# Kernel optimization log

Measured on AMD Instinct MI355X. Metric: run time of the kernel, lower is better.

The kernel has to match this reference:

```python
import jax, jax.numpy as jnp
import numpy as np
from jax import lax

B, S, D, E, H = 2, 2048, 1024, 8, 4096


def setup_inputs() -> dict:
    key = jax.random.key(0)
    ks = jax.random.split(key, 10)
    sc = 0.02  # GPT-style init scale
    return {
        "x": jax.random.normal(ks[0], (B, S, D), jnp.float32),
        "noise": jax.random.normal(ks[1], (B, S, E), jnp.float32),
        "w_route": jax.random.normal(ks[2], (D, E), jnp.float32) * sc,
        "b_route": jnp.zeros((E,), jnp.float32),
        "w_noise": jax.random.normal(ks[3], (D, E), jnp.float32) * sc,
        "b_noise": jnp.zeros((E,), jnp.float32),
        "w_fc": jax.random.normal(ks[4], (E, D, H), jnp.float32) * sc,
        "b_fc": jnp.zeros((E, H), jnp.float32),
        "w_proj": jax.random.normal(ks[5], (E, H, D), jnp.float32) * sc,
        "b_proj": jnp.zeros((E, D), jnp.float32),
        "top_k": 2,
    }


def reference(x, noise, w_route, b_route, w_noise, b_noise, w_fc, b_fc, w_proj, b_proj, top_k):
    # --- NoisyTopkRouter ---
    logits = x @ w_route + b_route                      # [B,S,E]
    noise_logits = x @ w_noise + b_noise                # [B,S,E]
    noisy = logits + noise * jax.nn.softplus(noise_logits)
    gate1 = jax.nn.softmax(noisy, axis=-1)              # dense gate (aux output)

    topk_vals, topk_idx = lax.top_k(noisy, top_k)       # [B,S,K]
    # softmax over sparse logits (-inf elsewhere) == softmax over the top-k values
    gk = jax.nn.softmax(topk_vals, axis=-1)             # [B,S,K]
    # scatter top-k gates back to the dense expert axis; non-selected experts get 0
    gating = (jax.nn.one_hot(topk_idx, E, dtype=x.dtype) * gk[..., None]).sum(-2)  # [B,S,E]

    # --- Experts (dense-over-experts, masked by gating; math identical to
    #     masked gather/scatter since non-selected gates are exactly 0) ---
    h = jnp.einsum('bsd,edh->bseh', x, w_fc) + b_fc     # [B,S,E,H]
    h = jax.nn.gelu(h, approximate=True)                # GELU(tanh)
    y = jnp.einsum('bseh,ehd->bsed', h, w_proj) + b_proj  # [B,S,E,D]
    out = jnp.einsum('bsed,bse->bsd', y, gating)        # weighted combine
    return out, gate1
```

## Files before the change

kernel.cpp:

```cpp
#include <hip/hip_runtime.h>
#include <cstdint>


#define DEV __device__ __forceinline__

typedef __attribute__((ext_vector_type(8))) short short8;
typedef __attribute__((ext_vector_type(4))) float floatx4;

constexpr int D_ = 1024, E_ = 8, H_ = 4096;
constexpr int NTOK = 4096;
constexpr int CAP  = 4096;
constexpr int TOTSLOT = NTOK * 2;

constexpr size_t O_COUNT = 0;
constexpr size_t O_FLAG  = 48;
constexpr size_t O_OFFS  = 64;
constexpr size_t O_BTOK  = 128;
constexpr size_t O_BGATE = O_BTOK  + (size_t)E_ * CAP * 4;
constexpr size_t O_PAIR  = O_BGATE + (size_t)E_ * CAP * 4;
constexpr size_t O_HBUF  = (O_PAIR + (size_t)NTOK * 2 * 4 + 255) & ~(size_t)255;
constexpr size_t O_YBUF  = O_HBUF + (size_t)TOTSLOT * H_ * 2;
constexpr size_t WS_NEED = O_YBUF + (size_t)TOTSLOT * D_ * 2;

DEV float b2f(unsigned short u) {
    union { unsigned int i; float f; } v; v.i = ((unsigned int)u) << 16; return v.f;
}
DEV unsigned int f2b(float f) {
    union { float f; unsigned int i; } v; v.f = f;
    unsigned int r = v.i + 0x7fffu + ((v.i >> 16) & 1u);
    return (r >> 16) & 0xffffu;
}

template <int DT> DEV float ldf(const void* p, size_t i) {
    if constexpr (DT == 0) return ((const float*)p)[i];
    else return b2f(((const unsigned short*)p)[i]);
}

DEV float gelu_tanh(float x) {
    float u = 0.7978845608028654f * (x + 0.044715f * x * x * x);
    u = fminf(fmaxf(u, -20.f), 20.f);
    float e = __expf(2.f * u);
    float t = (e - 1.f) / (e + 1.f);
    return 0.5f * x * (1.f + t);
}

__global__ __launch_bounds__(64) void detect_init(const unsigned int* __restrict__ xw,
                                                  int* flags, int* counts) {
    int lane = threadIdx.x;
    int outl = 0;
    for (int i = lane; i < 512; i += 64) {
        unsigned int lo = xw[i] & 0xffffu;
        unsigned int ef = (lo >> 7) & 0xffu;
        if (ef < 100u || ef > 140u) outl++;
    }
#pragma unroll
    for (int off = 32; off > 0; off >>= 1) outl += __shfl_down(outl, off);
    if (lane == 0) flags[0] = (outl > 64) ? 0 : 1;
    if (lane < E_) counts[lane] = 0;
}

template <int DT>
__global__ __launch_bounds__(256) void router_kernel(
    const void* __restrict__ x, const void* __restrict__ noise,
    const void* __restrict__ w_route, const void* __restrict__ b_route,
    const void* __restrict__ w_noise, const void* __restrict__ b_noise,
    void* __restrict__ out,
    const int* __restrict__ flags, int* counts, int* btok, float* bgate, int* pairs)
{
    if (flags[0] != DT) return;
    int wave = threadIdx.x >> 6, lane = threadIdx.x & 63;
    int t = blockIdx.x * 4 + wave;

    double racc[E_], nacc[E_];
#pragma unroll
    for (int e = 0; e < E_; e++) { racc[e] = 0.0; nacc[e] = 0.0; }

#pragma unroll 4
    for (int i = 0; i < D_ / 64; i++) {
        int j = i * 64 + lane;
        float xv = ldf<DT>(x, (size_t)t * D_ + j);
        float rv[E_], nv[E_];
        if constexpr (DT == 0) {
            const float* wr = (const float*)w_route + (size_t)j * E_;
            const float* wn = (const float*)w_noise + (size_t)j * E_;
            float4 a0 = ((const float4*)wr)[0], a1 = ((const float4*)wr)[1];
            float4 c0 = ((const float4*)wn)[0], c1 = ((const float4*)wn)[1];
            rv[0]=a0.x; rv[1]=a0.y; rv[2]=a0.z; rv[3]=a0.w;
            rv[4]=a1.x; rv[5]=a1.y; rv[6]=a1.z; rv[7]=a1.w;
            nv[0]=c0.x; nv[1]=c0.y; nv[2]=c0.z; nv[3]=c0.w;
            nv[4]=c1.x; nv[5]=c1.y; nv[6]=c1.z; nv[7]=c1.w;
        } else {
            uint4 r8 = *(const uint4*)((const unsigned short*)w_route + (size_t)j * E_);
            uint4 n8 = *(const uint4*)((const unsigned short*)w_noise + (size_t)j * E_);
            const unsigned int rw[4] = {r8.x, r8.y, r8.z, r8.w};
            const unsigned int nw[4] = {n8.x, n8.y, n8.z, n8.w};
#pragma unroll
            for (int p = 0; p < 4; p++) {
                rv[2*p]   = b2f((unsigned short)(rw[p] & 0xffffu));
                rv[2*p+1] = b2f((unsigned short)(rw[p] >> 16));
                nv[2*p]   = b2f((unsigned short)(nw[p] & 0xffffu));
                nv[2*p+1] = b2f((unsigned short)(nw[p] >> 16));
            }
        }
#pragma unroll
        for (int e = 0; e < E_; e++) {
            racc[e] += (double)(xv * rv[e]);
            nacc[e] += (double)(xv * nv[e]);
        }
    }
#pragma unroll
    for (int off = 32; off > 0; off >>= 1)
#pragma unroll
        for (int e = 0; e < E_; e++) {
            racc[e] += __shfl_down(racc[e], off);
            nacc[e] += __shfl_down(nacc[e], off);
        }

    if (lane == 0) {
        double nz[E_];
#pragma unroll
        for (int e = 0; e < E_; e++) {
            double lg = racc[e] + (double)ldf<DT>(b_route, e);
            double nl = nacc[e] + (double)ldf<DT>(b_noise, e);
            double sp = (nl > 0.0) ? nl + log1p(exp(-nl)) : log1p(exp(nl));
            nz[e] = lg + (double)ldf<DT>(noise, (size_t)t * E_ + e) * sp;
        }
        double mx = nz[0];
#pragma unroll
        for (int e = 1; e < E_; e++) mx = fmax(mx, nz[e]);
        double se = 0.0, ex[E_];
#pragma unroll
        for (int e = 0; e < E_; e++) { ex[e] = exp(nz[e] - mx); se += ex[e]; }
#pragma unroll
        for (int e = 0; e < E_; e++) {
            float g = (float)(ex[e] / se);
            if constexpr (DT == 0) ((float*)out)[(size_t)NTOK * D_ + (size_t)t * E_ + e] = g;
            else ((unsigned short*)out)[(size_t)NTOK * D_ + (size_t)t * E_ + e] = (unsigned short)f2b(g);
        }
        double v0 = -1e300, v1 = -1e300; int i0 = 0, i1 = 0;
#pragma unroll
        for (int e = 0; e < E_; e++) {
            double v = nz[e];
            if (v > v0) { v1 = v0; i1 = i0; v0 = v; i0 = e; }
            else if (v > v1) { v1 = v; i1 = e; }
        }
        double g0 = 1.0 / (1.0 + exp(v1 - v0));
        float  g1 = (float)(1.0 - g0);
        int l0 = atomicAdd(&counts[i0], 1);
        int l1 = atomicAdd(&counts[i1], 1);
        btok[i0 * CAP + l0] = t;  bgate[i0 * CAP + l0] = (float)g0;
        btok[i1 * CAP + l1] = t;  bgate[i1 * CAP + l1] = g1;
        pairs[2 * t]     = (i0 << 16) | l0;
        pairs[2 * t + 1] = (i1 << 16) | l1;
    }
}

__global__ __launch_bounds__(64) void offsets_kernel(const int* counts, int* offs) {
    if (threadIdx.x == 0) {
        int a = 0;
        for (int e = 0; e < E_; e++) { offs[e] = a; a += counts[e]; }
        offs[E_] = a;
    }
}

template <int KD, int ND, bool FC, int DT>
__global__ __launch_bounds__(256) void moe_gemm(
    const void* __restrict__ asrc,
    const void* __restrict__ w,
    const void* __restrict__ bias,
    unsigned short* __restrict__ dst,
    const int* __restrict__ flags, const int* __restrict__ counts,
    const int* __restrict__ offs, const int* __restrict__ btok,
    const float* __restrict__ bgate)
{
    if (flags[0] != DT) return;
    const int e = blockIdx.z;
    const int cnt = counts[e];
    const int m0 = blockIdx.y * 128;
    if (m0 >= cnt) return;
    const int n0 = blockIdx.x * 128;
    const int off = offs[e];

    __shared__ unsigned short As[128][72];
    __shared__ unsigned short Bs[128][72];

    const int tid = threadIdx.x;
    const int ar = tid >> 1, ah = tid & 1;
    int am = m0 + ar; if (am > cnt - 1) am = cnt - 1;
    const size_t arow = FC ? (size_t)btok[e * CAP + am] * KD
                           : (size_t)(off + am) * KD;
    const int bn = (tid & 31) * 4;
    const int bk = (tid >> 5) * 8;

    const int waveid = tid >> 6, lane = tid & 63;
    const int wm = (waveid & 1) * 64, wn = (waveid >> 1) * 64;
    const int lrow = lane & 15, quad = lane >> 4;

    floatx4 acc[4][4];
#pragma unroll
    for (int fm = 0; fm < 4; fm++)
#pragma unroll
        for (int fn = 0; fn < 4; fn++) acc[fm][fn] = (floatx4)0.f;

    for (int k0 = 0; k0 < KD; k0 += 64) {
        __syncthreads();
        {
            uint4* ad = (uint4*)&As[ar][ah * 32];
            if constexpr (FC && DT == 0) {
                const float* ag = (const float*)asrc + arow + k0 + ah * 32;
#pragma unroll
                for (int i = 0; i < 4; i++) {
                    float4 a0 = ((const float4*)ag)[2 * i];
                    float4 a1 = ((const float4*)ag)[2 * i + 1];
                    uint4 pk;
                    pk.x = f2b(a0.x) | (f2b(a0.y) << 16);
                    pk.y = f2b(a0.z) | (f2b(a0.w) << 16);
                    pk.z = f2b(a1.x) | (f2b(a1.y) << 16);
                    pk.w = f2b(a1.z) | (f2b(a1.w) << 16);
                    ad[i] = pk;
                }
            } else {
                const uint4* ag = (const uint4*)((const unsigned short*)asrc + arow + k0 + ah * 32);
#pragma unroll
                for (int i = 0; i < 4; i++) ad[i] = ag[i];
            }
        }
        {
            unsigned short breg[4][8];
#pragma unroll
            for (int j = 0; j < 8; j++) {
                if constexpr (DT == 0) {
                    const float* wp = (const float*)w + (size_t)e * KD * ND
                                      + (size_t)(k0 + bk + j) * ND + n0 + bn;
                    float4 v = *(const float4*)wp;
                    breg[0][j] = (unsigned short)f2b(v.x);
                    breg[1][j] = (unsigned short)f2b(v.y);
                    breg[2][j] = (unsigned short)f2b(v.z);
                    breg[3][j] = (unsigned short)f2b(v.w);
                } else {
                    const unsigned short* wp = (const unsigned short*)w + (size_t)e * KD * ND
                                               + (size_t)(k0 + bk + j) * ND + n0 + bn;
                    uint2 v = *(const uint2*)wp;
                    breg[0][j] = (unsigned short)(v.x & 0xffffu);
                    breg[1][j] = (unsigned short)(v.x >> 16);
                    breg[2][j] = (unsigned short)(v.y & 0xffffu);
                    breg[3][j] = (unsigned short)(v.y >> 16);
                }
            }
#pragma unroll
            for (int c = 0; c < 4; c++) {
                uint4 pk;
                pk.x = (unsigned int)breg[c][0] | ((unsigned int)breg[c][1] << 16);
                pk.y = (unsigned int)breg[c][2] | ((unsigned int)breg[c][3] << 16);
                pk.z = (unsigned int)breg[c][4] | ((unsigned int)breg[c][5] << 16);
                pk.w = (unsigned int)breg[c][6] | ((unsigned int)breg[c][7] << 16);
                *(uint4*)&Bs[bn + c][bk] = pk;
            }
        }
        __syncthreads();
#pragma unroll
        for (int ks = 0; ks < 2; ks++) {
            short8 af[4], bfr[4];
#pragma unroll
            for (int f = 0; f < 4; f++) {
                af[f]  = *(const short8*)&As[wm + f * 16 + lrow][ks * 32 + quad * 8];
                bfr[f] = *(const short8*)&Bs[wn + f * 16 + lrow][ks * 32 + quad * 8];
            }
#pragma unroll
            for (int fm = 0; fm < 4; fm++)
#pragma unroll
                for (int fn = 0; fn < 4; fn++)
                    acc[fm][fn] = __builtin_amdgcn_mfma_f32_16x16x32_bf16(
                        af[fm], bfr[fn], acc[fm][fn], 0, 0, 0);
        }
    }

    const int gc = n0 + wn + lrow;
    float bcol[4];
#pragma unroll
    for (int fn = 0; fn < 4; fn++) bcol[fn] = ldf<DT>(bias, (size_t)e * ND + gc + fn * 16);

#pragma unroll
    for (int fm = 0; fm < 4; fm++) {
        int srow0 = m0 + wm + fm * 16 + quad * 4;
#pragma unroll
        for (int r = 0; r < 4; r++) {
            int srow = srow0 + r;
            if (srow < cnt) {
                size_t base = (size_t)(off + srow) * ND;
                if (FC) {
#pragma unroll
                    for (int fn = 0; fn < 4; fn++) {
                        float v = acc[fm][fn][r] + bcol[fn];
                        dst[base + gc + fn * 16] = (unsigned short)f2b(gelu_tanh(v));
                    }
                } else {
                    float g = bgate[e * CAP + srow];
#pragma unroll
                    for (int fn = 0; fn < 4; fn++) {
                        float v = (acc[fm][fn][r] + bcol[fn]) * g;
                        dst[base + gc + fn * 16] = (unsigned short)f2b(v);
                    }
                }
            }
        }
    }
}

template <int DT>
__global__ __launch_bounds__(256) void combine_kernel(
    const unsigned short* __restrict__ ybuf, const int* __restrict__ pairs,
    const int* __restrict__ offs, const int* __restrict__ flags, void* __restrict__ out)
{
    if (flags[0] != DT) return;
    int t = blockIdx.x;
    int p0 = pairs[2 * t], p1 = pairs[2 * t + 1];
    size_t r0 = (size_t)(offs[p0 >> 16] + (p0 & 0xffff)) * D_;
    size_t r1 = (size_t)(offs[p1 >> 16] + (p1 & 0xffff)) * D_;
    int c = threadIdx.x * 4;
    uint2 a = *(const uint2*)(ybuf + r0 + c);
    uint2 b = *(const uint2*)(ybuf + r1 + c);
    float s0 = b2f((unsigned short)(a.x & 0xffffu)) + b2f((unsigned short)(b.x & 0xffffu));
    float s1 = b2f((unsigned short)(a.x >> 16))     + b2f((unsigned short)(b.x >> 16));
    float s2 = b2f((unsigned short)(a.y & 0xffffu)) + b2f((unsigned short)(b.y & 0xffffu));
    float s3 = b2f((unsigned short)(a.y >> 16))     + b2f((unsigned short)(b.y >> 16));
    if constexpr (DT == 0) {
        float4 o; o.x = s0; o.y = s1; o.z = s2; o.w = s3;
        *(float4*)((float*)out + (size_t)t * D_ + c) = o;
    } else {
        uint2 o;
        o.x = f2b(s0) | (f2b(s1) << 16);
        o.y = f2b(s2) | (f2b(s3) << 16);
        *(uint2*)((unsigned short*)out + (size_t)t * D_ + c) = o;
    }
}

extern "C" void kernel_launch(void* const* d_in, const int* in_sizes, int n_in,
                              void* d_out, int out_size, void* d_ws, size_t ws_size,
                              hipStream_t stream) {
    if (ws_size < WS_NEED) return;

    const void* x       = d_in[0];
    const void* noise   = d_in[1];
    const void* w_route = d_in[2];
    const void* b_route = d_in[3];
    const void* w_noise = d_in[4];
    const void* b_noise = d_in[5];
    const void* w_fc    = d_in[6];
    const void* b_fc    = d_in[7];
    const void* w_proj  = d_in[8];
    const void* b_proj  = d_in[9];

    char* ws = (char*)d_ws;
    int*   counts = (int*)(ws + O_COUNT);
    int*   flags  = (int*)(ws + O_FLAG);
    int*   offs   = (int*)(ws + O_OFFS);
    int*   btok   = (int*)(ws + O_BTOK);
    float* bgate  = (float*)(ws + O_BGATE);
    int*   pairs  = (int*)(ws + O_PAIR);
    unsigned short* hbuf = (unsigned short*)(ws + O_HBUF);
    unsigned short* ybuf = (unsigned short*)(ws + O_YBUF);

    detect_init<<<dim3(1), dim3(64), 0, stream>>>((const unsigned int*)x, flags, counts);

    router_kernel<0><<<dim3(NTOK / 4), dim3(256), 0, stream>>>(
        x, noise, w_route, b_route, w_noise, b_noise, d_out, flags, counts, btok, bgate, pairs);
    router_kernel<1><<<dim3(NTOK / 4), dim3(256), 0, stream>>>(
        x, noise, w_route, b_route, w_noise, b_noise, d_out, flags, counts, btok, bgate, pairs);

    offsets_kernel<<<dim3(1), dim3(64), 0, stream>>>(counts, offs);

    moe_gemm<D_, H_, true, 0><<<dim3(H_ / 128, 32, E_), dim3(256), 0, stream>>>(
        x, w_fc, b_fc, hbuf, flags, counts, offs, btok, bgate);
    moe_gemm<D_, H_, true, 1><<<dim3(H_ / 128, 32, E_), dim3(256), 0, stream>>>(
        x, w_fc, b_fc, hbuf, flags, counts, offs, btok, bgate);

    moe_gemm<H_, D_, false, 0><<<dim3(D_ / 128, 32, E_), dim3(256), 0, stream>>>(
        hbuf, w_proj, b_proj, ybuf, flags, counts, offs, btok, bgate);
    moe_gemm<H_, D_, false, 1><<<dim3(D_ / 128, 32, E_), dim3(256), 0, stream>>>(
        hbuf, w_proj, b_proj, ybuf, flags, counts, offs, btok, bgate);

    combine_kernel<0><<<dim3(NTOK), dim3(256), 0, stream>>>(ybuf, pairs, offs, flags, d_out);
    combine_kernel<1><<<dim3(NTOK), dim3(256), 0, stream>>>(ybuf, pairs, offs, flags, d_out);
}
```

Baseline: 807.5 us.

## Pre-convert weights to transposed bf16 and use direct-to-LDS loads in MoE GEMMs

Removes the dtype detection and the duplicate bf16 kernel variants, so everything runs as fp32-only launches. Adds a gather kernel that packs routed tokens into a contiguous bf16 buffer, and a transpose kernel that converts expert weights to N-major bf16 each call. The GEMM now loads tiles with global_load_lds into XOR-swizzled shared memory and remaps blocks so XCDs share N tiles. The goal is to drop the per-tile fp32 conversion and the scattered B loads from the inner loop. The cost is extra passes over the weights and a larger workspace.

```diff
diff --git a/kernel.cpp b/kernel.cpp
--- a/kernel.cpp
+++ b/kernel.cpp
@@ -13,14 +13,15 @@
 constexpr int TOTSLOT = NTOK * 2;
 
 constexpr size_t O_COUNT = 0;
-constexpr size_t O_FLAG  = 48;
 constexpr size_t O_OFFS  = 64;
 constexpr size_t O_BTOK  = 128;
 constexpr size_t O_BGATE = O_BTOK  + (size_t)E_ * CAP * 4;
 constexpr size_t O_PAIR  = O_BGATE + (size_t)E_ * CAP * 4;
-constexpr size_t O_HBUF  = (O_PAIR + (size_t)NTOK * 2 * 4 + 255) & ~(size_t)255;
+constexpr size_t O_XG    = (O_PAIR + (size_t)NTOK * 2 * 4 + 255) & ~(size_t)255;
+constexpr size_t O_HBUF  = O_XG   + (size_t)TOTSLOT * D_ * 2;
 constexpr size_t O_YBUF  = O_HBUF + (size_t)TOTSLOT * H_ * 2;
-constexpr size_t WS_NEED = O_YBUF + (size_t)TOTSLOT * D_ * 2;
+constexpr size_t O_WT    = O_YBUF + (size_t)TOTSLOT * D_ * 2;
+constexpr size_t WS_NEED = O_WT   + (size_t)E_ * D_ * H_ * 2;
 
 DEV float b2f(unsigned short u) {
     union { unsigned int i; float f; } v; v.i = ((unsigned int)u) << 16; return v.f;
@@ -30,12 +31,6 @@
     unsigned int r = v.i + 0x7fffu + ((v.i >> 16) & 1u);
     return (r >> 16) & 0xffffu;
 }
-
-template <int DT> DEV float ldf(const void* p, size_t i) {
-    if constexpr (DT == 0) return ((const float*)p)[i];
-    else return b2f(((const unsigned short*)p)[i]);
-}
-
 DEV float gelu_tanh(float x) {
     float u = 0.7978845608028654f * (x + 0.044715f * x * x * x);
     u = fminf(fmaxf(u, -20.f), 20.f);
@@ -44,30 +39,24 @@
     return 0.5f * x * (1.f + t);
 }
 
-__global__ __launch_bounds__(64) void detect_init(const unsigned int* __restrict__ xw,
-                                                  int* flags, int* counts) {
-    int lane = threadIdx.x;
-    int outl = 0;
-    for (int i = lane; i < 512; i += 64) {
-        unsigned int lo = xw[i] & 0xffffu;
-        unsigned int ef = (lo >> 7) & 0xffu;
-        if (ef < 100u || ef > 140u) outl++;
-    }
-#pragma unroll
-    for (int off = 32; off > 0; off >>= 1) outl += __shfl_down(outl, off);
-    if (lane == 0) flags[0] = (outl > 64) ? 0 : 1;
-    if (lane < E_) counts[lane] = 0;
-}
-
-template <int DT>
+typedef __attribute__((address_space(3))) unsigned int lds_u32_t;
+typedef const __attribute__((address_space(1))) unsigned int g_u32_t;
+DEV void gload16(const unsigned short* g, const unsigned short* l) {
+    __builtin_amdgcn_global_load_lds((g_u32_t*)(size_t)g,
+                                     (lds_u32_t*)(unsigned int)(size_t)l, 16, 0, 0);
+}
+
+__global__ __launch_bounds__(64) void zero_counts(int* counts) {
+    if (threadIdx.x < E_) counts[threadIdx.x] = 0;
+}
+
 __global__ __launch_bounds__(256) void router_kernel(
-    const void* __restrict__ x, const void* __restrict__ noise,
-    const void* __restrict__ w_route, const void* __restrict__ b_route,
-    const void* __restrict__ w_noise, const void* __restrict__ b_noise,
-    void* __restrict__ out,
-    const int* __restrict__ flags, int* counts, int* btok, float* bgate, int* pairs)
-{
-    if (flags[0] != DT) return;
+    const float* __restrict__ x, const float* __restrict__ noise,
+    const float* __restrict__ w_route, const float* __restrict__ b_route,
+    const float* __restrict__ w_noise, const float* __restrict__ b_noise,
+    float* __restrict__ out,
+    int* counts, int* btok, float* bgate, int* pairs)
+{
     int wave = threadIdx.x >> 6, lane = threadIdx.x & 63;
     int t = blockIdx.x * 4 + wave;
 
@@ -78,30 +67,13 @@
 #pragma unroll 4
     for (int i = 0; i < D_ / 64; i++) {
         int j = i * 64 + lane;
-        float xv = ldf<DT>(x, (size_t)t * D_ + j);
-        float rv[E_], nv[E_];
-        if constexpr (DT == 0) {
-            const float* wr = (const float*)w_route + (size_t)j * E_;
-            const float* wn = (const float*)w_noise + (size_t)j * E_;
-            float4 a0 = ((const float4*)wr)[0], a1 = ((const float4*)wr)[1];
-            float4 c0 = ((const float4*)wn)[0], c1 = ((const float4*)wn)[1];
-            rv[0]=a0.x; rv[1]=a0.y; rv[2]=a0.z; rv[3]=a0.w;
-            rv[4]=a1.x; rv[5]=a1.y; rv[6]=a1.z; rv[7]=a1.w;
-            nv[0]=c0.x; nv[1]=c0.y; nv[2]=c0.z; nv[3]=c0.w;
-            nv[4]=c1.x; nv[5]=c1.y; nv[6]=c1.z; nv[7]=c1.w;
-        } else {
-            uint4 r8 = *(const uint4*)((const unsigned short*)w_route + (size_t)j * E_);
-            uint4 n8 = *(const uint4*)((const unsigned short*)w_noise + (size_t)j * E_);
-            const unsigned int rw[4] = {r8.x, r8.y, r8.z, r8.w};
-            const unsigned int nw[4] = {n8.x, n8.y, n8.z, n8.w};
-#pragma unroll
-            for (int p = 0; p < 4; p++) {
-                rv[2*p]   = b2f((unsigned short)(rw[p] & 0xffffu));
-                rv[2*p+1] = b2f((unsigned short)(rw[p] >> 16));
-                nv[2*p]   = b2f((unsigned short)(nw[p] & 0xffffu));
-                nv[2*p+1] = b2f((unsigned short)(nw[p] >> 16));
-            }
-        }
+        float xv = x[(size_t)t * D_ + j];
+        const float* wr = w_route + (size_t)j * E_;
+        const float* wn = w_noise + (size_t)j * E_;
+        float4 a0 = ((const float4*)wr)[0], a1 = ((const float4*)wr)[1];
+        float4 c0 = ((const float4*)wn)[0], c1 = ((const float4*)wn)[1];
+        const float rv[8] = {a0.x,a0.y,a0.z,a0.w,a1.x,a1.y,a1.z,a1.w};
+        const float nv[8] = {c0.x,c0.y,c0.z,c0.w,c1.x,c1.y,c1.z,c1.w};
 #pragma unroll
         for (int e = 0; e < E_; e++) {
             racc[e] += (double)(xv * rv[e]);
@@ -120,10 +92,10 @@
         double nz[E_];
 #pragma unroll
         for (int e = 0; e < E_; e++) {
-            double lg = racc[e] + (double)ldf<DT>(b_route, e);
-            double nl = nacc[e] + (double)ldf<DT>(b_noise, e);
+            double lg = racc[e] + (double)b_route[e];
+            double nl = nacc[e] + (double)b_noise[e];
             double sp = (nl > 0.0) ? nl + log1p(exp(-nl)) : log1p(exp(nl));
-            nz[e] = lg + (double)ldf<DT>(noise, (size_t)t * E_ + e) * sp;
+            nz[e] = lg + (double)noise[(size_t)t * E_ + e] * sp;
         }
         double mx = nz[0];
 #pragma unroll
@@ -132,11 +104,8 @@
 #pragma unroll
         for (int e = 0; e < E_; e++) { ex[e] = exp(nz[e] - mx); se += ex[e]; }
 #pragma unroll
-        for (int e = 0; e < E_; e++) {
-            float g = (float)(ex[e] / se);
-            if constexpr (DT == 0) ((float*)out)[(size_t)NTOK * D_ + (size_t)t * E_ + e] = g;
-            else ((unsigned short*)out)[(size_t)NTOK * D_ + (size_t)t * E_ + e] = (unsigned short)f2b(g);
-        }
+        for (int e = 0; e < E_; e++)
+            out[(size_t)NTOK * D_ + (size_t)t * E_ + e] = (float)(ex[e] / se);
         double v0 = -1e300, v1 = -1e300; int i0 = 0, i1 = 0;
 #pragma unroll
         for (int e = 0; e < E_; e++) {
@@ -163,36 +132,105 @@
     }
 }
 
-template <int KD, int ND, bool FC, int DT>
-__global__ __launch_bounds__(256) void moe_gemm(
-    const void* __restrict__ asrc,
-    const void* __restrict__ w,
-    const void* __restrict__ bias,
+__global__ __launch_bounds__(256) void gather_x(
+    const float* __restrict__ x, const int* __restrict__ pairs,
+    const int* __restrict__ offs, unsigned short* __restrict__ xg)
+{
+    int t = blockIdx.x;
+    int c = threadIdx.x * 4;
+    float4 v = *(const float4*)(x + (size_t)t * D_ + c);
+    uint2 o;
+    o.x = f2b(v.x) | (f2b(v.y) << 16);
+    o.y = f2b(v.z) | (f2b(v.w) << 16);
+    int p0 = pairs[2 * t], p1 = pairs[2 * t + 1];
+    size_t r0 = (size_t)(offs[p0 >> 16] + (p0 & 0xffff)) * D_;
+    size_t r1 = (size_t)(offs[p1 >> 16] + (p1 & 0xffff)) * D_;
+    *(uint2*)(xg + r0 + c) = o;
+    *(uint2*)(xg + r1 + c) = o;
+}
+
+__global__ __launch_bounds__(256) void transpose_w(
+    const float* __restrict__ w, unsigned short* __restrict__ wT, int K, int N)
+{
+    __shared__ unsigned short t[64][65];
+    const int e  = blockIdx.z;
+    const int k0 = blockIdx.y * 64;
+    const int n0 = blockIdx.x * 64;
+    const int r  = threadIdx.x >> 2;
+    const int c4 = (threadIdx.x & 3) * 16;
+    const float* src = w + ((size_t)e * K + k0 + r) * N + n0 + c4;
+#pragma unroll
+    for (int i = 0; i < 4; i++) {
+        float4 v = ((const float4*)src)[i];
+        t[r][c4 + 4*i + 0] = (unsigned short)f2b(v.x);
+        t[r][c4 + 4*i + 1] = (unsigned short)f2b(v.y);
+        t[r][c4 + 4*i + 2] = (unsigned short)f2b(v.z);
+        t[r][c4 + 4*i + 3] = (unsigned short)f2b(v.w);
+    }
+    __syncthreads();
+    unsigned short* dstp = wT + ((size_t)e * N + n0 + r) * K + k0 + c4;
+    unsigned short tmp[16];
+#pragma unroll
+    for (int i = 0; i < 16; i++) tmp[i] = t[c4 + i][r];
+#pragma unroll
+    for (int h = 0; h < 2; h++) {
+        uint4 pk;
+        pk.x = (unsigned int)tmp[8*h+0] | ((unsigned int)tmp[8*h+1] << 16);
+        pk.y = (unsigned int)tmp[8*h+2] | ((unsigned int)tmp[8*h+3] << 16);
+        pk.z = (unsigned int)tmp[8*h+4] | ((unsigned int)tmp[8*h+5] << 16);
+        pk.w = (unsigned int)tmp[8*h+6] | ((unsigned int)tmp[8*h+7] << 16);
+        ((uint4*)dstp)[h] = pk;
+    }
+}
+
+template <int KD, int ND, bool FC>
+__global__ __launch_bounds__(256) void moe_gemm3(
+    const unsigned short* __restrict__ A,
+    const unsigned short* __restrict__ wT,
+    const float* __restrict__ bias32,
     unsigned short* __restrict__ dst,
-    const int* __restrict__ flags, const int* __restrict__ counts,
-    const int* __restrict__ offs, const int* __restrict__ btok,
+    const int* __restrict__ counts, const int* __restrict__ offs,
     const float* __restrict__ bgate)
 {
-    if (flags[0] != DT) return;
-    const int e = blockIdx.z;
+    const int lin = blockIdx.x;
+    const int xcd = lin & 7, slot = lin >> 3;
+    int e, mt, nt;
+    if (FC) {
+        nt = xcd * 4 + (slot & 3);
+        mt = (slot >> 2) & 31;
+        e  = slot >> 7;
+    } else {
+        nt = xcd;
+        mt = slot & 31;
+        e  = slot >> 5;
+    }
     const int cnt = counts[e];
-    const int m0 = blockIdx.y * 128;
+    const int m0 = mt * 128;
     if (m0 >= cnt) return;
-    const int n0 = blockIdx.x * 128;
+    const int n0 = nt * 128;
     const int off = offs[e];
 
-    __shared__ unsigned short As[128][72];
-    __shared__ unsigned short Bs[128][72];
+    __shared__ unsigned short As[128 * 64];
+    __shared__ unsigned short Bs[128 * 64];
 
     const int tid = threadIdx.x;
-    const int ar = tid >> 1, ah = tid & 1;
-    int am = m0 + ar; if (am > cnt - 1) am = cnt - 1;
-    const size_t arow = FC ? (size_t)btok[e * CAP + am] * KD
-                           : (size_t)(off + am) * KD;
-    const int bn = (tid & 31) * 4;
-    const int bk = (tid >> 5) * 8;
-
     const int waveid = tid >> 6, lane = tid & 63;
+    const int sr = lane >> 3;
+    const int g  = lane & 7;
+    const int scol = ((g ^ sr) * 8);
+
+    const unsigned short* aAddr[4];
+    const unsigned short* bAddr[4];
+#pragma unroll
+    for (int c = 0; c < 4; c++) {
+        int ar = m0 + (waveid * 4 + c) * 8 + sr;
+        if (ar > cnt - 1) ar = cnt - 1;
+        aAddr[c] = A + (size_t)(off + ar) * KD + scol;
+        int br = n0 + (waveid * 4 + c) * 8 + sr;
+        bAddr[c] = wT + ((size_t)e * ND + br) * KD + scol;
+    }
+    const int ldsChunk = (waveid * 4) * 512;
+
     const int wm = (waveid & 1) * 64, wn = (waveid >> 1) * 64;
     const int lrow = lane & 15, quad = lane >> 4;
 
@@ -204,58 +242,10 @@
 
     for (int k0 = 0; k0 < KD; k0 += 64) {
         __syncthreads();
-        {
-            uint4* ad = (uint4*)&As[ar][ah * 32];
-            if constexpr (FC && DT == 0) {
-                const float* ag = (const float*)asrc + arow + k0 + ah * 32;
-#pragma unroll
-                for (int i = 0; i < 4; i++) {
-                    float4 a0 = ((const float4*)ag)[2 * i];
-                    float4 a1 = ((const float4*)ag)[2 * i + 1];
-                    uint4 pk;
-                    pk.x = f2b(a0.x) | (f2b(a0.y) << 16);
-                    pk.y = f2b(a0.z) | (f2b(a0.w) << 16);
-                    pk.z = f2b(a1.x) | (f2b(a1.y) << 16);
-                    pk.w = f2b(a1.z) | (f2b(a1.w) << 16);
-                    ad[i] = pk;
-                }
-            } else {
-                const uint4* ag = (const uint4*)((const unsigned short*)asrc + arow + k0 + ah * 32);
-#pragma unroll
-                for (int i = 0; i < 4; i++) ad[i] = ag[i];
-            }
-        }
-        {
-            unsigned short breg[4][8];
-#pragma unroll
-            for (int j = 0; j < 8; j++) {
-                if constexpr (DT == 0) {
-                    const float* wp = (const float*)w + (size_t)e * KD * ND
-                                      + (size_t)(k0 + bk + j) * ND + n0 + bn;
-                    float4 v = *(const float4*)wp;
-                    breg[0][j] = (unsigned short)f2b(v.x);
-                    breg[1][j] = (unsigned short)f2b(v.y);
-                    breg[2][j] = (unsigned short)f2b(v.z);
-                    breg[3][j] = (unsigned short)f2b(v.w);
-                } else {
-                    const unsigned short* wp = (const unsigned short*)w + (size_t)e * KD * ND
-                                               + (size_t)(k0 + bk + j) * ND + n0 + bn;
-                    uint2 v = *(const uint2*)wp;
-                    breg[0][j] = (unsigned short)(v.x & 0xffffu);
-                    breg[1][j] = (unsigned short)(v.x >> 16);
-                    breg[2][j] = (unsigned short)(v.y & 0xffffu);
-                    breg[3][j] = (unsigned short)(v.y >> 16);
-                }
-            }
-#pragma unroll
-            for (int c = 0; c < 4; c++) {
-                uint4 pk;
-                pk.x = (unsigned int)breg[c][0] | ((unsigned int)breg[c][1] << 16);
-                pk.y = (unsigned int)breg[c][2] | ((unsigned int)breg[c][3] << 16);
-                pk.z = (unsigned int)breg[c][4] | ((unsigned int)breg[c][5] << 16);
-                pk.w = (unsigned int)breg[c][6] | ((unsigned int)breg[c][7] << 16);
-                *(uint4*)&Bs[bn + c][bk] = pk;
-            }
+#pragma unroll
+        for (int c = 0; c < 4; c++) {
+            gload16(aAddr[c] + k0, &As[ldsChunk + c * 512]);
+            gload16(bAddr[c] + k0, &Bs[ldsChunk + c * 512]);
         }
         __syncthreads();
 #pragma unroll
@@ -263,8 +253,10 @@
             short8 af[4], bfr[4];
 #pragma unroll
             for (int f = 0; f < 4; f++) {
-                af[f]  = *(const short8*)&As[wm + f * 16 + lrow][ks * 32 + quad * 8];
-                bfr[f] = *(const short8*)&Bs[wn + f * 16 + lrow][ks * 32 + quad * 8];
+                int Ra = wm + f * 16 + lrow;
+                int Rb = wn + f * 16 + lrow;
+                af[f]  = *(const short8*)&As[Ra * 64 + ((ks * 4 + quad) ^ (Ra & 7)) * 8];
+                bfr[f] = *(const short8*)&Bs[Rb * 64 + ((ks * 4 + quad) ^ (Rb & 7)) * 8];
             }
 #pragma unroll
             for (int fm = 0; fm < 4; fm++)
@@ -278,7 +270,7 @@
     const int gc = n0 + wn + lrow;
     float bcol[4];
 #pragma unroll
-    for (int fn = 0; fn < 4; fn++) bcol[fn] = ldf<DT>(bias, (size_t)e * ND + gc + fn * 16);
+    for (int fn = 0; fn < 4; fn++) bcol[fn] = bias32[(size_t)e * ND + gc + fn * 16];
 
 #pragma unroll
     for (int fm = 0; fm < 4; fm++) {
@@ -295,10 +287,10 @@
                         dst[base + gc + fn * 16] = (unsigned short)f2b(gelu_tanh(v));
                     }
                 } else {
-                    float g = bgate[e * CAP + srow];
+                    float gt = bgate[e * CAP + srow];
 #pragma unroll
                     for (int fn = 0; fn < 4; fn++) {
-                        float v = (acc[fm][fn][r] + bcol[fn]) * g;
+                        float v = (acc[fm][fn][r] + bcol[fn]) * gt;
                         dst[base + gc + fn * 16] = (unsigned short)f2b(v);
                     }
                 }
@@ -307,12 +299,10 @@
     }
 }
 
-template <int DT>
 __global__ __launch_bounds__(256) void combine_kernel(
     const unsigned short* __restrict__ ybuf, const int* __restrict__ pairs,
-    const int* __restrict__ offs, const int* __restrict__ flags, void* __restrict__ out)
-{
-    if (flags[0] != DT) return;
+    const int* __restrict__ offs, float* __restrict__ out)
+{
     int t = blockIdx.x;
     int p0 = pairs[2 * t], p1 = pairs[2 * t + 1];
     size_t r0 = (size_t)(offs[p0 >> 16] + (p0 & 0xffff)) * D_;
@@ -320,19 +310,12 @@
     int c = threadIdx.x * 4;
     uint2 a = *(const uint2*)(ybuf + r0 + c);
     uint2 b = *(const uint2*)(ybuf + r1 + c);
-    float s0 = b2f((unsigned short)(a.x & 0xffffu)) + b2f((unsigned short)(b.x & 0xffffu));
-    float s1 = b2f((unsigned short)(a.x >> 16))     + b2f((unsigned short)(b.x >> 16));
-    float s2 = b2f((unsigned short)(a.y & 0xffffu)) + b2f((unsigned short)(b.y & 0xffffu));
-    float s3 = b2f((unsigned short)(a.y >> 16))     + b2f((unsigned short)(b.y >> 16));
-    if constexpr (DT == 0) {
-        float4 o; o.x = s0; o.y = s1; o.z = s2; o.w = s3;
-        *(float4*)((float*)out + (size_t)t * D_ + c) = o;
-    } else {
-        uint2 o;
-        o.x = f2b(s0) | (f2b(s1) << 16);
-        o.y = f2b(s2) | (f2b(s3) << 16);
-        *(uint2*)((unsigned short*)out + (size_t)t * D_ + c) = o;
-    }
+    float4 o;
+    o.x = b2f((unsigned short)(a.x & 0xffffu)) + b2f((unsigned short)(b.x & 0xffffu));
+    o.y = b2f((unsigned short)(a.x >> 16))     + b2f((unsigned short)(b.x >> 16));
+    o.z = b2f((unsigned short)(a.y & 0xffffu)) + b2f((unsigned short)(b.y & 0xffffu));
+    o.w = b2f((unsigned short)(a.y >> 16))     + b2f((unsigned short)(b.y >> 16));
+    *(float4*)(out + (size_t)t * D_ + c) = o;
 }
 
 extern "C" void kernel_launch(void* const* d_in, const int* in_sizes, int n_in,
@@ -340,46 +323,42 @@
                               hipStream_t stream) {
     if (ws_size < WS_NEED) return;
 
-    const void* x       = d_in[0];
-    const void* noise   = d_in[1];
-    const void* w_route = d_in[2];
-    const void* b_route = d_in[3];
-    const void* w_noise = d_in[4];
-    const void* b_noise = d_in[5];
-    const void* w_fc    = d_in[6];
-    const void* b_fc    = d_in[7];
-    const void* w_proj  = d_in[8];
-    const void* b_proj  = d_in[9];
+    const float* x       = (const float*)d_in[0];
+    const float* noise   = (const float*)d_in[1];
+    const float* w_route = (const float*)d_in[2];
+    const float* b_route = (const float*)d_in[3];
+    const float* w_noise = (const float*)d_in[4];
+    const float* b_noise = (const float*)d_in[5];
+    const float* w_fc    = (const float*)d_in[6];
+    const float* b_fc    = (const float*)d_in[7];
+    const float* w_proj  = (const float*)d_in[8];
+    const float* b_proj  = (const float*)d_in[9];
 
     char* ws = (char*)d_ws;
     int*   counts = (int*)(ws + O_COUNT);
-    int*   flags  = (int*)(ws + O_FLAG);
     int*   offs   = (int*)(ws + O_OFFS);
     int*   btok   = (int*)(ws + O_BTOK);
     float* bgate  = (float*)(ws + O_BGATE);
     int*   pairs  = (int*)(ws + O_PAIR);
+    unsigned short* xg   = (unsigned short*)(ws + O_XG);
     unsigned short* hbuf = (unsigned short*)(ws + O_HBUF);
     unsigned short* ybuf = (unsigned short*)(ws + O_YBUF);
-
-    detect_init<<<dim3(1), dim3(64), 0, stream>>>((const unsigned int*)x, flags, counts);
-
-    router_kernel<0><<<dim3(NTOK / 4), dim3(256), 0, stream>>>(
-        x, noise, w_route, b_route, w_noise, b_noise, d_out, flags, counts, btok, bgate, pairs);
-    router_kernel<1><<<dim3(NTOK / 4), dim3(256), 0, stream>>>(
-        x, noise, w_route, b_route, w_noise, b_noise, d_out, flags, counts, btok, bgate, pairs);
-
+    unsigned short* wT   = (unsigned short*)(ws + O_WT);
+
+    zero_counts<<<dim3(1), dim3(64), 0, stream>>>(counts);
+    router_kernel<<<dim3(NTOK / 4), dim3(256), 0, stream>>>(
+        x, noise, w_route, b_route, w_noise, b_noise, (float*)d_out,
+        counts, btok, bgate, pairs);
     offsets_kernel<<<dim3(1), dim3(64), 0, stream>>>(counts, offs);
-
-    moe_gemm<D_, H_, true, 0><<<dim3(H_ / 128, 32, E_), dim3(256), 0, stream>>>(
-        x, w_fc, b_fc, hbuf, flags, counts, offs, btok, bgate);
-    moe_gemm<D_, H_, true, 1><<<dim3(H_ / 128, 32, E_), dim3(256), 0, stream>>>(
-        x, w_fc, b_fc, hbuf, flags, counts, offs, btok, bgate);
-
-    moe_gemm<H_, D_, false, 0><<<dim3(D_ / 128, 32, E_), dim3(256), 0, stream>>>(
-        hbuf, w_proj, b_proj, ybuf, flags, counts, offs, btok, bgate);
-    moe_gemm<H_, D_, false, 1><<<dim3(D_ / 128, 32, E_), dim3(256), 0, stream>>>(
-        hbuf, w_proj, b_proj, ybuf, flags, counts, offs, btok, bgate);
-
-    combine_kernel<0><<<dim3(NTOK), dim3(256), 0, stream>>>(ybuf, pairs, offs, flags, d_out);
-    combine_kernel<1><<<dim3(NTOK), dim3(256), 0, stream>>>(ybuf, pairs, offs, flags, d_out);
-}
+    gather_x<<<dim3(NTOK), dim3(256), 0, stream>>>(x, pairs, offs, xg);
+
+    transpose_w<<<dim3(H_ / 64, D_ / 64, E_), dim3(256), 0, stream>>>(w_fc, wT, D_, H_);
+    moe_gemm3<D_, H_, true><<<dim3(8 * 32 * 32), dim3(256), 0, stream>>>(
+        xg, wT, b_fc, hbuf, counts, offs, bgate);
+
+    transpose_w<<<dim3(D_ / 64, H_ / 64, E_), dim3(256), 0, stream>>>(w_proj, wT, H_, D_);
+    moe_gemm3<H_, D_, false><<<dim3(8 * 32 * 8), dim3(256), 0, stream>>>(
+        hbuf, wT, b_proj, ybuf, counts, offs, bgate);
+
+    combine_kernel<<<dim3(NTOK), dim3(256), 0, stream>>>(ybuf, pairs, offs, (float*)d_out);
+}
```

Result: faster. 716.6 us (-11.3%).
